# Kernel tuning notes

Hardware: AMD Instinct MI355X
Metric: run time of the kernel (lower is better)

The kernel has to match this reference:

```python
import jax, jax.numpy as jnp
import numpy as np

BATCH, T, HID = 4, 2048, 1024
H = P = 1024  # input_dim and ssm_size (expand_ratio=1.0)
EPS = 1e-5
DISCRETIZATION = "IM"  # 'IM' or 'IMEX'


def setup_inputs() -> dict:
    key = jax.random.key(0)
    ks = jax.random.split(key, 10)
    std_b = 1.0 / np.sqrt(H)
    std_c = 1.0 / np.sqrt(P)
    u = lambda k, s, lo, hi: jax.random.uniform(k, s, jnp.float32, lo, hi)
    return {
        "hidden_states": jax.random.normal(ks[0], (BATCH, T, HID), jnp.float32),
        "Wi": jax.random.normal(ks[1], (H, HID), jnp.float32) / np.sqrt(HID),
        "Wg": jax.random.normal(ks[2], (H, HID), jnp.float32) / np.sqrt(HID),
        "Wo": jax.random.normal(ks[3], (HID, H), jnp.float32) / np.sqrt(H),
        "A_diag": u(ks[4], (P,), 0.0, 1.0),
        "B_param": u(ks[5], (P, H, 2), -std_b, std_b),
        "C_param": u(ks[6], (H, P, 2), -std_c, std_c),
        "D": jax.random.normal(ks[7], (H,), jnp.float32),
        "dt": u(ks[8], (P,), 0.0, 1.0),
        "norm_weight": jnp.ones((H,), jnp.float32),
    }


def _linoss(x, B_param, C_param, A_diag, dt_p, D):
    """LinOSS oscillatory SSM recurrence with complex B/C and diagonal A.
    x: (B,T,H) real input. State z,y in C^P (re/im stacked on last axis)."""
    A = jax.nn.relu(A_diag)       # (P,) nonneg frequencies
    dt = jax.nn.sigmoid(dt_p)     # (P,) timesteps in (0,1)
    # Bu_{re,im}[b,t,p] = sum_h x[b,t,h] * B_{re,im}[p,h]
    Bu = jnp.einsum('bth,phc->btpc', x, B_param)  # (B,T,P,2)
    if DISCRETIZATION == "IM":
        S = 1.0 / (1.0 + dt * dt * A)
        m11, m12, m21, m22 = S, -dt * A * S, dt * S, S
        f1, f2 = dt * S, dt * dt * S
    else:  # IMEX
        one = jnp.ones_like(dt)
        m11, m12, m21, m22 = one, -dt * A, dt, 1.0 - dt * dt * A
        f1, f2 = dt, dt * dt
    c = lambda v: v[None, :, None]  # broadcast (P,) -> (B,P,2)

    def step(carry, bu):
        z, y = carry  # each (B,P,2)
        z1 = c(m11) * z + c(m12) * y + c(f1) * bu
        y1 = c(m21) * z + c(m22) * y + c(f2) * bu
        return (z1, y1), y1

    z0 = jnp.zeros((x.shape[0], A.shape[0], 2), x.dtype)
    _, ys = jax.lax.scan(step, (z0, z0), jnp.swapaxes(Bu, 0, 1))
    ys = jnp.swapaxes(ys, 0, 1)  # (B,T,P,2)
    # o = Re(C @ y) + D * x
    o = (jnp.einsum('btp,hp->bth', ys[..., 0], C_param[..., 0])
         - jnp.einsum('btp,hp->bth', ys[..., 1], C_param[..., 1]))
    return o + x * D


def reference(hidden_states, Wi, Wg, Wo, A_diag, B_param, C_param, D, dt, norm_weight):
    x = hidden_states @ Wi.T                        # i_proj
    o = _linoss(x, B_param, C_param, A_diag, dt, D)  # fused_recurrent_linoss
    g = hidden_states @ Wg.T                        # g_proj
    # FusedRMSNormGated: rmsnorm(o) * weight * swish(g)
    o = o * jax.lax.rsqrt(jnp.mean(o * o, axis=-1, keepdims=True) + EPS) * norm_weight
    o = o * (g * jax.nn.sigmoid(g))
    return o @ Wo.T                                  # o_proj
```

## Files before the change

### kernel.cpp

```cpp
#include <hip/hip_runtime.h>
#include <hip/hip_bf16.h>
#include <math.h>

#define BB 4
#define TT 2048
#define HH 1024
#define PP 1024
#define MT 8192
#define C2 2048
#define NC 64
#define LCH 32

typedef __attribute__((ext_vector_type(8))) short  bf16x8;
typedef __attribute__((ext_vector_type(4))) float  f32x4;

__device__ __forceinline__ ushort f2bf(float f) {
    union { float f; unsigned u; } v; v.f = f;
    unsigned r = v.u + 0x7fffu + ((v.u >> 16) & 1u);
    return (ushort)(r >> 16);
}
__device__ __forceinline__ float bf2f(ushort h) {
    union { unsigned u; float f; } v; v.u = ((unsigned)h) << 16;
    return v.f;
}

__device__ __forceinline__ void gload16(const ushort* g, ushort* l) {
    __builtin_amdgcn_global_load_lds((const __attribute__((address_space(1))) void*)g,
                                     (__attribute__((address_space(3))) void*)l,
                                     16, 0, 0);
}

__device__ __forceinline__ void barrier_raw() { __builtin_amdgcn_s_barrier(); }
__device__ __forceinline__ void lgk0() { asm volatile("s_waitcnt lgkmcnt(0)" ::: "memory"); }
__device__ __forceinline__ void vm6()  { asm volatile("s_waitcnt vmcnt(6)"   ::: "memory"); }
__device__ __forceinline__ void vm0()  { asm volatile("s_waitcnt vmcnt(0)"   ::: "memory"); }

__global__ void f32_to_bf16_k(const float* __restrict__ s, ushort* __restrict__ d) {
    int i = blockIdx.x * 256 + threadIdx.x;
    float4 v = ((const float4*)s)[i];
    ushort4 o;
    o.x = f2bf(v.x); o.y = f2bf(v.y); o.z = f2bf(v.z); o.w = f2bf(v.w);
    ((ushort4*)d)[i] = o;
}

__global__ void repack_B_bf(const float* __restrict__ src, ushort* __restrict__ dst) {
    int idx = blockIdx.x * 256 + threadIdx.x;
    int p = idx >> 10;
    int h = idx & 1023;
    float2 v = ((const float2*)src)[idx];
    dst[(size_t)p * HH + h]        = f2bf(v.x);
    dst[(size_t)(p + PP) * HH + h] = f2bf(v.y);
}

__global__ void repack_C_bf(const float* __restrict__ src, ushort* __restrict__ dst) {
    int idx = blockIdx.x * 256 + threadIdx.x;
    int h = idx >> 10;
    int p = idx & 1023;
    float2 v = ((const float2*)src)[idx];
    dst[(size_t)h * C2 + p]      = f2bf(v.x);
    dst[(size_t)h * C2 + PP + p] = f2bf(-v.y);
}

template<int BM, int STORE_BF16>
__global__ __launch_bounds__(512, 2) void gemm8p(
    const ushort* __restrict__ A, int lda,
    const ushort* __restrict__ B, int ldb,
    void* __restrict__ Cp, int ldc, int K, int nbx)
{
    constexpr int BN  = 256;
    constexpr int MR  = BM / 32;
    constexpr int MRH = MR / 2;
    constexpr int TA  = BM * 128;
    constexpr int TB  = BN * 128;
    __shared__ __align__(16) char smem[2 * TA + 2 * TB];

    const int bid = blockIdx.x;
    const int cpx = gridDim.x >> 3;
    const int wg  = (bid & 7) * cpx + (bid >> 3);
    const int by  = wg / nbx;
    const int bx  = wg - by * nbx;
    const int bm  = by * BM;
    const int bn  = bx * BN;

    const int tid  = threadIdx.x;
    const int wave = tid >> 6;
    const int lane = tid & 63;
    const int wr   = wave >> 2;
    const int wc   = wave & 3;
    const int lr   = lane & 15;
    const int kg   = lane >> 4;

    const int e  = (wave << 10) + ((lane << 4) ^ (((lane >> 5) & 1) << 5));
    const int r0 = e >> 7;
    const int c0 = (e & 127) >> 1;

    auto stA = [&](int bi, int u, int kt) {
        gload16(A + (size_t)(bm + u * 64 + r0) * lda + kt * 64 + c0,
                (ushort*)(smem + bi * TA + u * 8192 + (wave << 10)));
    };
    auto stB = [&](int bi, int u, int kt) {
        gload16(B + (size_t)(bn + u * 64 + r0) * ldb + kt * 64 + c0,
                (ushort*)(smem + 2 * TA + bi * TB + u * 8192 + (wave << 10)));
    };

    bf16x8 Af[MRH][2], Bf[4][2];
    auto ldsA = [&](int bi, int qm) {
#pragma unroll
        for (int f = 0; f < MRH; ++f)
#pragma unroll
            for (int kk = 0; kk < 2; ++kk) {
                int row = wr * (BM / 2) + qm * (BM / 4) + f * 16 + lr;
                int o = row * 128 + kk * 64 + kg * 16;
                o ^= ((o >> 9) & 1) << 5;
                Af[f][kk] = *(const bf16x8*)(smem + bi * TA + o);
            }
    };
    auto ldsB = [&](int bi) {
#pragma unroll
        for (int n = 0; n < 4; ++n)
#pragma unroll
            for (int kk = 0; kk < 2; ++kk) {
                int row = wc * 64 + n * 16 + lr;
                int o = row * 128 + kk * 64 + kg * 16;
                o ^= ((o >> 9) & 1) << 5;
                Bf[n][kk] = *(const bf16x8*)(smem + 2 * TA + bi * TB + o);
            }
    };

    f32x4 acc[MR][4];
#pragma unroll
    for (int m = 0; m < MR; ++m)
#pragma unroll
        for (int n = 0; n < 4; ++n)
#pragma unroll
            for (int i = 0; i < 4; ++i) acc[m][n][i] = 0.f;

    auto mfma16 = [&](int qm, int qn) {
        __builtin_amdgcn_s_setprio(1);
#pragma unroll
        for (int f = 0; f < MRH; ++f)
#pragma unroll
            for (int n2 = 0; n2 < 2; ++n2)
#pragma unroll
                for (int kk = 0; kk < 2; ++kk)
                    acc[qm * MRH + f][qn * 2 + n2] =
                        __builtin_amdgcn_mfma_f32_16x16x32_bf16(
                            Af[f][kk], Bf[qn * 2 + n2][kk],
                            acc[qm * MRH + f][qn * 2 + n2], 0, 0, 0);
        __builtin_amdgcn_s_setprio(0);
    };

    if constexpr (BM == 256) {
        stA(0, 0, 0); stA(0, 1, 0); stA(0, 2, 0); stA(0, 3, 0);
        stB(0, 0, 0); stB(0, 1, 0); stB(0, 2, 0); stB(0, 3, 0);
        stB(1, 0, 1); stB(1, 1, 1); stB(1, 2, 1); stB(1, 3, 1);
        stA(1, 0, 1); stA(1, 2, 1);
    } else {
        stA(0, 0, 0); stA(0, 1, 0);
        stB(0, 0, 0); stB(0, 1, 0); stB(0, 2, 0); stB(0, 3, 0);
        stA(1, 0, 1); stA(1, 1, 1);
        stB(1, 0, 1); stB(1, 1, 1); stB(1, 2, 1); stB(1, 3, 1);
    }
    vm6();
    barrier_raw();

    const int nIter = K >> 7;
    for (int J = 0; J < nIter; ++J) {
        const bool pf  = (J + 1 < nIter);
        const int  kt1 = 2 * J + 1, kt2 = 2 * J + 2, kt3 = 2 * J + 3;
        ldsA(0, 0); ldsB(0);
        if constexpr (BM == 256) { stA(1, 1, kt1); stA(1, 3, kt1); }
        barrier_raw(); lgk0(); mfma16(0, 0); barrier_raw();
        if (pf) { stB(0, 0, kt2); stB(0, 1, kt2); }
        barrier_raw(); lgk0(); mfma16(0, 1); barrier_raw();
        ldsA(0, 1);
        if (pf) { stB(0, 2, kt2); stB(0, 3, kt2); }
        barrier_raw(); lgk0(); mfma16(1, 0); barrier_raw();
        if (pf) {
            if constexpr (BM == 256) { stA(0, 0, kt2); stA(0, 2, kt2); }
            else                     { stA(0, 0, kt2); stA(0, 1, kt2); }
        }
        barrier_raw(); lgk0(); mfma16(1, 1);
        if (pf) vm6(); else vm0();
        barrier_raw();
        ldsA(1, 0); ldsB(1);
        if constexpr (BM == 256) { if (pf) { stA(0, 1, kt2); stA(0, 3, kt2); } }
        barrier_raw(); lgk0(); mfma16(0, 0); barrier_raw();
        if (pf) { stB(1, 0, kt3); stB(1, 1, kt3); }
        barrier_raw(); lgk0(); mfma16(0, 1); barrier_raw();
        ldsA(1, 1);
        if (pf) { stB(1, 2, kt3); stB(1, 3, kt3); }
        barrier_raw(); lgk0(); mfma16(1, 0); barrier_raw();
        if (pf) {
            if constexpr (BM == 256) { stA(1, 0, kt3); stA(1, 2, kt3); }
            else                     { stA(1, 0, kt3); stA(1, 1, kt3); }
        }
        barrier_raw(); lgk0(); mfma16(1, 1);
        if (pf) vm6(); else vm0();
        barrier_raw();
    }

#pragma unroll
    for (int mf = 0; mf < MR; ++mf) {
#pragma unroll
        for (int n = 0; n < 4; ++n) {
            int col = bn + wc * 64 + n * 16 + lr;
#pragma unroll
            for (int i = 0; i < 4; ++i) {
                int row = bm + wr * (BM / 2) + mf * 16 + kg * 4 + i;
                float v = acc[mf][n][i];
                if (STORE_BF16)
                    ((ushort*)Cp)[(size_t)row * ldc + col] = f2bf(v);
                else
                    ((float*)Cp)[(size_t)row * ldc + col]  = v;
            }
        }
    }
}

__device__ __forceinline__ void linoss_coeffs(const float* A_diag, const float* dt_p,
                                              int p, float& m11, float& m12,
                                              float& m21, float& m22,
                                              float& f1, float& f2) {
    float A  = fmaxf(A_diag[p], 0.f);
    float dt = 1.f / (1.f + expf(-dt_p[p]));
    float S  = 1.f / (1.f + dt * dt * A);
    m11 = S;        m12 = -dt * A * S;
    m21 = dt * S;   m22 = S;
    f1  = dt * S;   f2  = dt * dt * S;
}

__global__ void scan_passA(const float* __restrict__ Bu,
                           const float* __restrict__ A_diag,
                           const float* __restrict__ dt_p,
                           float2* __restrict__ sEnd) {
    int c = blockIdx.x * 256 + threadIdx.x;
    int b = blockIdx.y;
    int j = blockIdx.z;
    float m11, m12, m21, m22, f1, f2;
    linoss_coeffs(A_diag, dt_p, c & 1023, m11, m12, m21, m22, f1, f2);
    const float* bu = Bu + ((size_t)(b * TT + j * LCH)) * C2 + c;
    float z = 0.f, y = 0.f;
#pragma unroll 8
    for (int i = 0; i < LCH; ++i) {
        float u  = bu[(size_t)i * C2];
        float z1 = m11 * z + m12 * y + f1 * u;
        float y1 = m21 * z + m22 * y + f2 * u;
        z = z1; y = y1;
    }
    sEnd[((size_t)j * BB + b) * C2 + c] = make_float2(z, y);
}

__global__ void scan_combine(const float* __restrict__ A_diag,
                             const float* __restrict__ dt_p,
                             const float2* __restrict__ sEnd,
                             float2* __restrict__ sInit) {
    int idx = blockIdx.x * 256 + threadIdx.x;
    int c = idx & (C2 - 1);
    int b = idx >> 11;
    float m11, m12, m21, m22, f1, f2;
    linoss_coeffs(A_diag, dt_p, c & 1023, m11, m12, m21, m22, f1, f2);
    float e11 = m11, e12 = m12, e21 = m21, e22 = m22;
#pragma unroll
    for (int s = 0; s < 5; ++s) {
        float n11 = e11 * e11 + e12 * e21;
        float n12 = e11 * e12 + e12 * e22;
        float n21 = e21 * e11 + e22 * e21;
        float n22 = e21 * e12 + e22 * e22;
        e11 = n11; e12 = n12; e21 = n21; e22 = n22;
    }
    float z = 0.f, y = 0.f;
    for (int j = 0; j < NC; ++j) {
        size_t off = ((size_t)j * BB + b) * C2 + c;
        sInit[off] = make_float2(z, y);
        float2 le = sEnd[off];
        float z1 = e11 * z + e12 * y + le.x;
        float y1 = e21 * z + e22 * y + le.y;
        z = z1; y = y1;
    }
}

__global__ void scan_passB(const float* __restrict__ Bu,
                           const float* __restrict__ A_diag,
                           const float* __restrict__ dt_p,
                           const float2* __restrict__ sInit,
                           ushort* __restrict__ YSb) {
    int c = blockIdx.x * 256 + threadIdx.x;
    int b = blockIdx.y;
    int j = blockIdx.z;
    float m11, m12, m21, m22, f1, f2;
    linoss_coeffs(A_diag, dt_p, c & 1023, m11, m12, m21, m22, f1, f2);
    float2 s0 = sInit[((size_t)j * BB + b) * C2 + c];
    float z = s0.x, y = s0.y;
    const float* bu = Bu  + ((size_t)(b * TT + j * LCH)) * C2 + c;
    ushort*      ys = YSb + ((size_t)(b * TT + j * LCH)) * C2 + c;
#pragma unroll 8
    for (int i = 0; i < LCH; ++i) {
        float u  = bu[(size_t)i * C2];
        float z1 = m11 * z + m12 * y + f1 * u;
        float y1 = m21 * z + m22 * y + f2 * u;
        z = z1; y = y1;
        ys[(size_t)i * C2] = f2bf(y);
    }
}

__global__ void rmsgate_kernel(const float* __restrict__ O,
                               const ushort* __restrict__ XGb,
                               const float* __restrict__ Dv,
                               const float* __restrict__ nw,
                               ushort* __restrict__ V) {
    int m = blockIdx.x;
    int t = threadIdx.x;
    float4  o4 = ((const float4*)(O + (size_t)m * HH))[t];
    ushort4 x4 = ((const ushort4*)(XGb + (size_t)m * C2))[t];
    float4  d4 = ((const float4*)Dv)[t];
    float of[4];
    of[0] = o4.x + d4.x * bf2f(x4.x);
    of[1] = o4.y + d4.y * bf2f(x4.y);
    of[2] = o4.z + d4.z * bf2f(x4.z);
    of[3] = o4.w + d4.w * bf2f(x4.w);
    float ss = of[0]*of[0] + of[1]*of[1] + of[2]*of[2] + of[3]*of[3];
#pragma unroll
    for (int o = 32; o > 0; o >>= 1) ss += __shfl_down(ss, o);
    __shared__ float wsum[4];
    if ((t & 63) == 0) wsum[t >> 6] = ss;
    __syncthreads();
    float tot = wsum[0] + wsum[1] + wsum[2] + wsum[3];
    float r = rsqrtf(tot * (1.f / (float)HH) + 1e-5f);

    ushort4 g4 = ((const ushort4*)(XGb + (size_t)m * C2 + HH))[t];
    float4  w4 = ((const float4*)nw)[t];
    float g[4] = {bf2f(g4.x), bf2f(g4.y), bf2f(g4.z), bf2f(g4.w)};
    float w[4] = {w4.x, w4.y, w4.z, w4.w};
    ushort4 vout;
    ushort* vo = &vout.x;
#pragma unroll
    for (int i = 0; i < 4; ++i) {
        float sw = g[i] / (1.f + expf(-g[i]));
        vo[i] = f2bf(of[i] * r * w[i] * sw);
    }
    ((ushort4*)(V + (size_t)m * HH))[t] = vout;
}

extern "C" void kernel_launch(void* const* d_in, const int* in_sizes, int n_in,
                              void* d_out, int out_size, void* d_ws, size_t ws_size,
                              hipStream_t stream) {
    const float* hs      = (const float*)d_in[0];
    const float* Wi      = (const float*)d_in[1];
    const float* Wg      = (const float*)d_in[2];
    const float* Wo      = (const float*)d_in[3];
    const float* A_diag  = (const float*)d_in[4];
    const float* B_param = (const float*)d_in[5];
    const float* C_param = (const float*)d_in[6];
    const float* Dv      = (const float*)d_in[7];
    const float* dtp     = (const float*)d_in[8];
    const float* nw      = (const float*)d_in[9];
    float* out = (float*)d_out;

    char* ws = (char*)d_ws;
    ushort* hsb  = (ushort*)ws;                                   ws += (size_t)MT * HH * 2;
    ushort* Wigb = (ushort*)ws;                                   ws += (size_t)C2 * HH * 2;
    ushort* Wob  = (ushort*)ws;                                   ws += (size_t)HH * HH * 2;
    ushort* Bpkb = (ushort*)ws;                                   ws += (size_t)C2 * HH * 2;
    ushort* Cpkb = (ushort*)ws;                                   ws += (size_t)HH * C2 * 2;
    ushort* XGb  = (ushort*)ws;                                   ws += (size_t)MT * C2 * 2;
    float*  Bu   = (float*)ws;                                    ws += (size_t)MT * C2 * 4;
    ushort* YSb  = (ushort*)ws;                                   ws += (size_t)MT * C2 * 2;
    float*  O    = (float*)ws;                                    ws += (size_t)MT * HH * 4;
    ushort* Vb   = (ushort*)ws;                                   ws += (size_t)MT * HH * 2;
    float2* sEnd  = (float2*)ws;                                  ws += (size_t)NC * BB * C2 * 8;
    float2* sInit = (float2*)ws;

    dim3 blk(256);

    f32_to_bf16_k<<<dim3((MT * HH) / 1024), blk, 0, stream>>>(hs, hsb);
    f32_to_bf16_k<<<dim3((HH * HH) / 1024), blk, 0, stream>>>(Wi, Wigb);
    f32_to_bf16_k<<<dim3((HH * HH) / 1024), blk, 0, stream>>>(Wg, Wigb + (size_t)HH * HH);
    f32_to_bf16_k<<<dim3((HH * HH) / 1024), blk, 0, stream>>>(Wo, Wob);
    repack_B_bf<<<dim3((PP * HH) / 256), blk, 0, stream>>>(B_param, Bpkb);
    repack_C_bf<<<dim3((HH * PP) / 256), blk, 0, stream>>>(C_param, Cpkb);

    gemm8p<256, 1><<<dim3(256), dim3(512), 0, stream>>>(
        hsb, HH, Wigb, HH, XGb, C2, HH, 8);

    gemm8p<256, 0><<<dim3(256), dim3(512), 0, stream>>>(
        XGb, C2, Bpkb, HH, Bu, C2, HH, 8);

    scan_passA<<<dim3(C2 / 256, BB, NC), blk, 0, stream>>>(Bu, A_diag, dtp, sEnd);
    scan_combine<<<dim3((BB * C2) / 256), blk, 0, stream>>>(A_diag, dtp, sEnd, sInit);
    scan_passB<<<dim3(C2 / 256, BB, NC), blk, 0, stream>>>(Bu, A_diag, dtp, sInit, YSb);

    gemm8p<128, 0><<<dim3(256), dim3(512), 0, stream>>>(
        YSb, C2, Cpkb, C2, O, HH, C2, 4);

    rmsgate_kernel<<<dim3(MT), blk, 0, stream>>>(O, XGb, Dv, nw, Vb);

    gemm8p<128, 0><<<dim3(256), dim3(512), 0, stream>>>(
        Vb, HH, Wob, HH, out, HH, HH, 4);
}
```

Baseline: 229.2 us.

## Software-pipeline GEMM LDS reads, fix swizzle, store Bu in bf16, fuse conversions

The GEMM main loop is restructured so LDS fragment loads for the next quarter-step are issued before the current MFMA batch. It uses two A-fragment register sets, split B loads and fewer barriers, and changes the LDS XOR swizzle to a per-row 8-way pattern to cut bank conflicts. Separately, the Bu intermediate is written as bf16 instead of fp32, which halves the scan's read traffic at some precision cost. The four fp32-to-bf16 conversion launches are also merged into one kernel. The extra register buffers raise register pressure, and the looser vmcnt waits need correct ordering.

```diff
diff --git a/kernel.cpp b/kernel.cpp
--- a/kernel.cpp
+++ b/kernel.cpp
@@ -29,18 +29,31 @@
                                      (__attribute__((address_space(3))) void*)l,
                                      16, 0, 0);
 }
-
 __device__ __forceinline__ void barrier_raw() { __builtin_amdgcn_s_barrier(); }
 __device__ __forceinline__ void lgk0() { asm volatile("s_waitcnt lgkmcnt(0)" ::: "memory"); }
+__device__ __forceinline__ void vm4()  { asm volatile("s_waitcnt vmcnt(4)"   ::: "memory"); }
 __device__ __forceinline__ void vm6()  { asm volatile("s_waitcnt vmcnt(6)"   ::: "memory"); }
 __device__ __forceinline__ void vm0()  { asm volatile("s_waitcnt vmcnt(0)"   ::: "memory"); }
 
-__global__ void f32_to_bf16_k(const float* __restrict__ s, ushort* __restrict__ d) {
+__global__ void convert_all(const float* __restrict__ hs, const float* __restrict__ Wi,
+                            const float* __restrict__ Wg, const float* __restrict__ Wo,
+                            ushort* __restrict__ hsb, ushort* __restrict__ Wigb,
+                            ushort* __restrict__ Wob) {
     int i = blockIdx.x * 256 + threadIdx.x;
-    float4 v = ((const float4*)s)[i];
+    const int HS4 = MT * HH / 4;
+    const int W4  = HH * HH / 4;
+    const float4* s;
+    ushort4* d;
+    if (i < HS4)               { s = (const float4*)hs + i;               d = (ushort4*)hsb  + i; }
+    else if (i < HS4 + 2 * W4) { int j = i - HS4;
+                                 s = (const float4*)(j < W4 ? Wi : Wg) + (j < W4 ? j : j - W4);
+                                 d = (ushort4*)Wigb + j; }
+    else                       { int j = i - HS4 - 2 * W4;
+                                 s = (const float4*)Wo + j;               d = (ushort4*)Wob + j; }
+    float4 v = *s;
     ushort4 o;
     o.x = f2bf(v.x); o.y = f2bf(v.y); o.z = f2bf(v.z); o.w = f2bf(v.w);
-    ((ushort4*)d)[i] = o;
+    *d = o;
 }
 
 __global__ void repack_B_bf(const float* __restrict__ src, ushort* __restrict__ dst) {
@@ -90,7 +103,7 @@
     const int lr   = lane & 15;
     const int kg   = lane >> 4;
 
-    const int e  = (wave << 10) + ((lane << 4) ^ (((lane >> 5) & 1) << 5));
+    const int e  = (wave << 10) + ((lane << 4) ^ (((lane >> 3) & 7) << 4));
     const int r0 = e >> 7;
     const int c0 = (e & 127) >> 1;
 
@@ -103,39 +116,39 @@
                 (ushort*)(smem + 2 * TA + bi * TB + u * 8192 + (wave << 10)));
     };
 
-    bf16x8 Af[MRH][2], Bf[4][2];
-    auto ldsA = [&](int bi, int qm) {
+    bf16x8 Af0[MRH][2], Af1[MRH][2], Bf[4][2];
+    auto ldsA = [&](int bi, int qm, bf16x8 (&Af)[MRH][2]) {
 #pragma unroll
         for (int f = 0; f < MRH; ++f)
 #pragma unroll
             for (int kk = 0; kk < 2; ++kk) {
                 int row = wr * (BM / 2) + qm * (BM / 4) + f * 16 + lr;
                 int o = row * 128 + kk * 64 + kg * 16;
-                o ^= ((o >> 9) & 1) << 5;
+                o ^= (row & 7) << 4;
                 Af[f][kk] = *(const bf16x8*)(smem + bi * TA + o);
             }
     };
-    auto ldsB = [&](int bi) {
+    auto ldsBh = [&](int bi, int h) {
+#pragma unroll
+        for (int n = 0; n < 2; ++n)
+#pragma unroll
+            for (int kk = 0; kk < 2; ++kk) {
+                int row = wc * 64 + (h * 2 + n) * 16 + lr;
+                int o = row * 128 + kk * 64 + kg * 16;
+                o ^= (row & 7) << 4;
+                Bf[h * 2 + n][kk] = *(const bf16x8*)(smem + 2 * TA + bi * TB + o);
+            }
+    };
+
+    f32x4 acc[MR][4];
+#pragma unroll
+    for (int m = 0; m < MR; ++m)
 #pragma unroll
         for (int n = 0; n < 4; ++n)
 #pragma unroll
-            for (int kk = 0; kk < 2; ++kk) {
-                int row = wc * 64 + n * 16 + lr;
-                int o = row * 128 + kk * 64 + kg * 16;
-                o ^= ((o >> 9) & 1) << 5;
-                Bf[n][kk] = *(const bf16x8*)(smem + 2 * TA + bi * TB + o);
-            }
-    };
-
-    f32x4 acc[MR][4];
-#pragma unroll
-    for (int m = 0; m < MR; ++m)
-#pragma unroll
-        for (int n = 0; n < 4; ++n)
-#pragma unroll
             for (int i = 0; i < 4; ++i) acc[m][n][i] = 0.f;
 
-    auto mfma16 = [&](int qm, int qn) {
+    auto M = [&](bf16x8 (&Af)[MRH][2], int qm, int qn) {
         __builtin_amdgcn_s_setprio(1);
 #pragma unroll
         for (int f = 0; f < MRH; ++f)
@@ -158,47 +171,50 @@
     } else {
         stA(0, 0, 0); stA(0, 1, 0);
         stB(0, 0, 0); stB(0, 1, 0); stB(0, 2, 0); stB(0, 3, 0);
+        stB(1, 0, 1); stB(1, 1, 1); stB(1, 2, 1); stB(1, 3, 1);
         stA(1, 0, 1); stA(1, 1, 1);
-        stB(1, 0, 1); stB(1, 1, 1); stB(1, 2, 1); stB(1, 3, 1);
-    }
-    vm6();
-    barrier_raw();
+    }
+    vm6(); barrier_raw();
+    ldsA(0, 0, Af0); ldsBh(0, 1);
 
     const int nIter = K >> 7;
-    for (int J = 0; J < nIter; ++J) {
-        const bool pf  = (J + 1 < nIter);
-        const int  kt1 = 2 * J + 1, kt2 = 2 * J + 2, kt3 = 2 * J + 3;
-        ldsA(0, 0); ldsB(0);
+    auto iter = [&](int J, bool pf) {
+        const int kt1 = 2 * J + 1, kt2 = 2 * J + 2, kt3 = 2 * J + 3;
         if constexpr (BM == 256) { stA(1, 1, kt1); stA(1, 3, kt1); }
-        barrier_raw(); lgk0(); mfma16(0, 0); barrier_raw();
+        ldsBh(0, 0);
+        M(Af0, 0, 1);
+        lgk0(); barrier_raw();
         if (pf) { stB(0, 0, kt2); stB(0, 1, kt2); }
-        barrier_raw(); lgk0(); mfma16(0, 1); barrier_raw();
-        ldsA(0, 1);
+        ldsA(0, 1, Af1);
+        M(Af0, 0, 0);
         if (pf) { stB(0, 2, kt2); stB(0, 3, kt2); }
-        barrier_raw(); lgk0(); mfma16(1, 0); barrier_raw();
+        M(Af1, 1, 1);
+        lgk0(); if (pf) vm4(); else vm0(); barrier_raw();
         if (pf) {
             if constexpr (BM == 256) { stA(0, 0, kt2); stA(0, 2, kt2); }
             else                     { stA(0, 0, kt2); stA(0, 1, kt2); }
         }
-        barrier_raw(); lgk0(); mfma16(1, 1);
-        if (pf) vm6(); else vm0();
-        barrier_raw();
-        ldsA(1, 0); ldsB(1);
-        if constexpr (BM == 256) { if (pf) { stA(0, 1, kt2); stA(0, 3, kt2); } }
-        barrier_raw(); lgk0(); mfma16(0, 0); barrier_raw();
+        ldsA(1, 0, Af0); ldsBh(1, 1);
+        M(Af1, 1, 0);
+        if (pf) { if constexpr (BM == 256) { stA(0, 1, kt2); stA(0, 3, kt2); } }
+        ldsBh(1, 0);
+        M(Af0, 0, 1);
+        lgk0(); barrier_raw();
         if (pf) { stB(1, 0, kt3); stB(1, 1, kt3); }
-        barrier_raw(); lgk0(); mfma16(0, 1); barrier_raw();
-        ldsA(1, 1);
+        ldsA(1, 1, Af1);
+        M(Af0, 0, 0);
         if (pf) { stB(1, 2, kt3); stB(1, 3, kt3); }
-        barrier_raw(); lgk0(); mfma16(1, 0); barrier_raw();
+        M(Af1, 1, 1);
+        lgk0(); if (pf) vm4(); barrier_raw();
         if (pf) {
             if constexpr (BM == 256) { stA(1, 0, kt3); stA(1, 2, kt3); }
             else                     { stA(1, 0, kt3); stA(1, 1, kt3); }
+            ldsA(0, 0, Af0); ldsBh(0, 1);
         }
-        barrier_raw(); lgk0(); mfma16(1, 1);
-        if (pf) vm6(); else vm0();
-        barrier_raw();
-    }
+        M(Af1, 1, 0);
+    };
+    for (int J = 0; J < nIter - 1; ++J) iter(J, true);
+    iter(nIter - 1, false);
 
 #pragma unroll
     for (int mf = 0; mf < MR; ++mf) {
@@ -230,7 +246,7 @@
     f1  = dt * S;   f2  = dt * dt * S;
 }
 
-__global__ void scan_passA(const float* __restrict__ Bu,
+__global__ void scan_passA(const ushort* __restrict__ Bu,
                            const float* __restrict__ A_diag,
                            const float* __restrict__ dt_p,
                            float2* __restrict__ sEnd) {
@@ -239,11 +255,11 @@
     int j = blockIdx.z;
     float m11, m12, m21, m22, f1, f2;
     linoss_coeffs(A_diag, dt_p, c & 1023, m11, m12, m21, m22, f1, f2);
-    const float* bu = Bu + ((size_t)(b * TT + j * LCH)) * C2 + c;
+    const ushort* bu = Bu + ((size_t)(b * TT + j * LCH)) * C2 + c;
     float z = 0.f, y = 0.f;
 #pragma unroll 8
     for (int i = 0; i < LCH; ++i) {
-        float u  = bu[(size_t)i * C2];
+        float u  = bf2f(bu[(size_t)i * C2]);
         float z1 = m11 * z + m12 * y + f1 * u;
         float y1 = m21 * z + m22 * y + f2 * u;
         z = z1; y = y1;
@@ -280,7 +296,7 @@
     }
 }
 
-__global__ void scan_passB(const float* __restrict__ Bu,
+__global__ void scan_passB(const ushort* __restrict__ Bu,
                            const float* __restrict__ A_diag,
                            const float* __restrict__ dt_p,
                            const float2* __restrict__ sInit,
@@ -292,11 +308,11 @@
     linoss_coeffs(A_diag, dt_p, c & 1023, m11, m12, m21, m22, f1, f2);
     float2 s0 = sInit[((size_t)j * BB + b) * C2 + c];
     float z = s0.x, y = s0.y;
-    const float* bu = Bu  + ((size_t)(b * TT + j * LCH)) * C2 + c;
-    ushort*      ys = YSb + ((size_t)(b * TT + j * LCH)) * C2 + c;
+    const ushort* bu = Bu  + ((size_t)(b * TT + j * LCH)) * C2 + c;
+    ushort*       ys = YSb + ((size_t)(b * TT + j * LCH)) * C2 + c;
 #pragma unroll 8
     for (int i = 0; i < LCH; ++i) {
-        float u  = bu[(size_t)i * C2];
+        float u  = bf2f(bu[(size_t)i * C2]);
         float z1 = m11 * z + m12 * y + f1 * u;
         float y1 = m21 * z + m22 * y + f2 * u;
         z = z1; y = y1;
@@ -364,7 +380,7 @@
     ushort* Bpkb = (ushort*)ws;                                   ws += (size_t)C2 * HH * 2;
     ushort* Cpkb = (ushort*)ws;                                   ws += (size_t)HH * C2 * 2;
     ushort* XGb  = (ushort*)ws;                                   ws += (size_t)MT * C2 * 2;
-    float*  Bu   = (float*)ws;                                    ws += (size_t)MT * C2 * 4;
+    ushort* Bu   = (ushort*)ws;                                   ws += (size_t)MT * C2 * 2;
     ushort* YSb  = (ushort*)ws;                                   ws += (size_t)MT * C2 * 2;
     float*  O    = (float*)ws;                                    ws += (size_t)MT * HH * 4;
     ushort* Vb   = (ushort*)ws;                                   ws += (size_t)MT * HH * 2;
@@ -373,17 +389,15 @@
 
     dim3 blk(256);
 
-    f32_to_bf16_k<<<dim3((MT * HH) / 1024), blk, 0, stream>>>(hs, hsb);
-    f32_to_bf16_k<<<dim3((HH * HH) / 1024), blk, 0, stream>>>(Wi, Wigb);
-    f32_to_bf16_k<<<dim3((HH * HH) / 1024), blk, 0, stream>>>(Wg, Wigb + (size_t)HH * HH);
-    f32_to_bf16_k<<<dim3((HH * HH) / 1024), blk, 0, stream>>>(Wo, Wob);
+    convert_all<<<dim3((MT * HH / 4 + 3 * HH * HH / 4) / 256), blk, 0, stream>>>(
+        hs, Wi, Wg, Wo, hsb, Wigb, Wob);
     repack_B_bf<<<dim3((PP * HH) / 256), blk, 0, stream>>>(B_param, Bpkb);
     repack_C_bf<<<dim3((HH * PP) / 256), blk, 0, stream>>>(C_param, Cpkb);
 
     gemm8p<256, 1><<<dim3(256), dim3(512), 0, stream>>>(
         hsb, HH, Wigb, HH, XGb, C2, HH, 8);
 
-    gemm8p<256, 0><<<dim3(256), dim3(512), 0, stream>>>(
+    gemm8p<256, 1><<<dim3(256), dim3(512), 0, stream>>>(
         XGb, C2, Bpkb, HH, Bu, C2, HH, 8);
 
     scan_passA<<<dim3(C2 / 256, BB, NC), blk, 0, stream>>>(Bu, A_diag, dtp, sEnd);
```

After: 332.5 us. +45.1%, slower.

## Store Bu in bf16, merge conversion launches, and change LDS swizzle pattern

Applied to the files above, without the earlier changes.

Combines the four fp32-to-bf16 conversion launches into a single kernel, cutting launch overhead. The Bu GEMM now writes bf16 output, and both scan passes read bf16, halving Bu write and read traffic at the cost of precision in the recurrence input. The GEMM shared-memory XOR swizzle changes from a single-bit swap to a row-based 3-bit swizzle, aiming to reduce LDS bank conflicts. The lower-precision Bu may add error that accumulates through the scan.

```diff
diff --git a/kernel.cpp b/kernel.cpp
--- a/kernel.cpp
+++ b/kernel.cpp
@@ -29,18 +29,30 @@
                                      (__attribute__((address_space(3))) void*)l,
                                      16, 0, 0);
 }
-
 __device__ __forceinline__ void barrier_raw() { __builtin_amdgcn_s_barrier(); }
 __device__ __forceinline__ void lgk0() { asm volatile("s_waitcnt lgkmcnt(0)" ::: "memory"); }
 __device__ __forceinline__ void vm6()  { asm volatile("s_waitcnt vmcnt(6)"   ::: "memory"); }
 __device__ __forceinline__ void vm0()  { asm volatile("s_waitcnt vmcnt(0)"   ::: "memory"); }
 
-__global__ void f32_to_bf16_k(const float* __restrict__ s, ushort* __restrict__ d) {
+__global__ void convert_all(const float* __restrict__ hs, const float* __restrict__ Wi,
+                            const float* __restrict__ Wg, const float* __restrict__ Wo,
+                            ushort* __restrict__ hsb, ushort* __restrict__ Wigb,
+                            ushort* __restrict__ Wob) {
     int i = blockIdx.x * 256 + threadIdx.x;
-    float4 v = ((const float4*)s)[i];
+    const int HS4 = MT * HH / 4;
+    const int W4  = HH * HH / 4;
+    const float4* s;
+    ushort4* d;
+    if (i < HS4)               { s = (const float4*)hs + i;               d = (ushort4*)hsb  + i; }
+    else if (i < HS4 + 2 * W4) { int j = i - HS4;
+                                 s = (const float4*)(j < W4 ? Wi : Wg) + (j < W4 ? j : j - W4);
+                                 d = (ushort4*)Wigb + j; }
+    else                       { int j = i - HS4 - 2 * W4;
+                                 s = (const float4*)Wo + j;               d = (ushort4*)Wob + j; }
+    float4 v = *s;
     ushort4 o;
     o.x = f2bf(v.x); o.y = f2bf(v.y); o.z = f2bf(v.z); o.w = f2bf(v.w);
-    ((ushort4*)d)[i] = o;
+    *d = o;
 }
 
 __global__ void repack_B_bf(const float* __restrict__ src, ushort* __restrict__ dst) {
@@ -90,7 +102,7 @@
     const int lr   = lane & 15;
     const int kg   = lane >> 4;
 
-    const int e  = (wave << 10) + ((lane << 4) ^ (((lane >> 5) & 1) << 5));
+    const int e  = (wave << 10) + ((lane << 4) ^ (((lane >> 3) & 7) << 4));
     const int r0 = e >> 7;
     const int c0 = (e & 127) >> 1;
 
@@ -111,7 +123,7 @@
             for (int kk = 0; kk < 2; ++kk) {
                 int row = wr * (BM / 2) + qm * (BM / 4) + f * 16 + lr;
                 int o = row * 128 + kk * 64 + kg * 16;
-                o ^= ((o >> 9) & 1) << 5;
+                o ^= (row & 7) << 4;
                 Af[f][kk] = *(const bf16x8*)(smem + bi * TA + o);
             }
     };
@@ -122,7 +134,7 @@
             for (int kk = 0; kk < 2; ++kk) {
                 int row = wc * 64 + n * 16 + lr;
                 int o = row * 128 + kk * 64 + kg * 16;
-                o ^= ((o >> 9) & 1) << 5;
+                o ^= (row & 7) << 4;
                 Bf[n][kk] = *(const bf16x8*)(smem + 2 * TA + bi * TB + o);
             }
     };
@@ -230,7 +242,7 @@
     f1  = dt * S;   f2  = dt * dt * S;
 }
 
-__global__ void scan_passA(const float* __restrict__ Bu,
+__global__ void scan_passA(const ushort* __restrict__ Bu,
                            const float* __restrict__ A_diag,
                            const float* __restrict__ dt_p,
                            float2* __restrict__ sEnd) {
@@ -239,11 +251,11 @@
     int j = blockIdx.z;
     float m11, m12, m21, m22, f1, f2;
     linoss_coeffs(A_diag, dt_p, c & 1023, m11, m12, m21, m22, f1, f2);
-    const float* bu = Bu + ((size_t)(b * TT + j * LCH)) * C2 + c;
+    const ushort* bu = Bu + ((size_t)(b * TT + j * LCH)) * C2 + c;
     float z = 0.f, y = 0.f;
 #pragma unroll 8
     for (int i = 0; i < LCH; ++i) {
-        float u  = bu[(size_t)i * C2];
+        float u  = bf2f(bu[(size_t)i * C2]);
         float z1 = m11 * z + m12 * y + f1 * u;
         float y1 = m21 * z + m22 * y + f2 * u;
         z = z1; y = y1;
@@ -280,7 +292,7 @@
     }
 }
 
-__global__ void scan_passB(const float* __restrict__ Bu,
+__global__ void scan_passB(const ushort* __restrict__ Bu,
                            const float* __restrict__ A_diag,
                            const float* __restrict__ dt_p,
                            const float2* __restrict__ sInit,
@@ -292,11 +304,11 @@
     linoss_coeffs(A_diag, dt_p, c & 1023, m11, m12, m21, m22, f1, f2);
     float2 s0 = sInit[((size_t)j * BB + b) * C2 + c];
     float z = s0.x, y = s0.y;
-    const float* bu = Bu  + ((size_t)(b * TT + j * LCH)) * C2 + c;
-    ushort*      ys = YSb + ((size_t)(b * TT + j * LCH)) * C2 + c;
+    const ushort* bu = Bu  + ((size_t)(b * TT + j * LCH)) * C2 + c;
+    ushort*       ys = YSb + ((size_t)(b * TT + j * LCH)) * C2 + c;
 #pragma unroll 8
     for (int i = 0; i < LCH; ++i) {
-        float u  = bu[(size_t)i * C2];
+        float u  = bf2f(bu[(size_t)i * C2]);
         float z1 = m11 * z + m12 * y + f1 * u;
         float y1 = m21 * z + m22 * y + f2 * u;
         z = z1; y = y1;
@@ -364,7 +376,7 @@
     ushort* Bpkb = (ushort*)ws;                                   ws += (size_t)C2 * HH * 2;
     ushort* Cpkb = (ushort*)ws;                                   ws += (size_t)HH * C2 * 2;
     ushort* XGb  = (ushort*)ws;                                   ws += (size_t)MT * C2 * 2;
-    float*  Bu   = (float*)ws;                                    ws += (size_t)MT * C2 * 4;
+    ushort* Bu   = (ushort*)ws;                                   ws += (size_t)MT * C2 * 2;
     ushort* YSb  = (ushort*)ws;                                   ws += (size_t)MT * C2 * 2;
     float*  O    = (float*)ws;                                    ws += (size_t)MT * HH * 4;
     ushort* Vb   = (ushort*)ws;                                   ws += (size_t)MT * HH * 2;
@@ -373,17 +385,15 @@
 
     dim3 blk(256);
 
-    f32_to_bf16_k<<<dim3((MT * HH) / 1024), blk, 0, stream>>>(hs, hsb);
-    f32_to_bf16_k<<<dim3((HH * HH) / 1024), blk, 0, stream>>>(Wi, Wigb);
-    f32_to_bf16_k<<<dim3((HH * HH) / 1024), blk, 0, stream>>>(Wg, Wigb + (size_t)HH * HH);
-    f32_to_bf16_k<<<dim3((HH * HH) / 1024), blk, 0, stream>>>(Wo, Wob);
+    convert_all<<<dim3((MT * HH / 4 + 3 * HH * HH / 4) / 256), blk, 0, stream>>>(
+        hs, Wi, Wg, Wo, hsb, Wigb, Wob);
     repack_B_bf<<<dim3((PP * HH) / 256), blk, 0, stream>>>(B_param, Bpkb);
     repack_C_bf<<<dim3((HH * PP) / 256), blk, 0, stream>>>(C_param, Cpkb);
 
     gemm8p<256, 1><<<dim3(256), dim3(512), 0, stream>>>(
         hsb, HH, Wigb, HH, XGb, C2, HH, 8);
 
-    gemm8p<256, 0><<<dim3(256), dim3(512), 0, stream>>>(
+    gemm8p<256, 1><<<dim3(256), dim3(512), 0, stream>>>(
         XGb, C2, Bpkb, HH, Bu, C2, HH, 8);
 
     scan_passA<<<dim3(C2 / 256, BB, NC), blk, 0, stream>>>(Bu, A_diag, dtp, sEnd);
```

Result: faster. 196.5 us (-14.3%).
